# Optimization experiments

Measured on AMD Instinct MI355X. Metric: run time of the kernel, lower is better.

Reference implementation:

```python
import jax, jax.numpy as jnp
import numpy as np

C = 1024
KSIZE = 7
PAD = 3
STRIDE = 1


def _dwconv(x, w):
    # x: [B, C, L], w: [C, 1, K] depthwise (feature_group_count=C)
    return jax.lax.conv_general_dilated(
        x, w,
        window_strides=(STRIDE,),
        padding=[(PAD, PAD)],
        feature_group_count=C,
        dimension_numbers=('NCH', 'OIH', 'NCH'),
    )


def setup_inputs() -> dict:
    key = jax.random.key(0)
    kx, kq, kk, kv = jax.random.split(key, 4)
    B, L = 8, 4096
    x = jax.random.normal(kx, (B, C, L), dtype=jnp.float32)
    # depthwise conv weights, fan_in = 1*K per group -> kaiming-ish scale
    scale = 1.0 / np.sqrt(KSIZE)
    q_w = jax.random.normal(kq, (C, 1, KSIZE), dtype=jnp.float32) * scale
    k_w = jax.random.normal(kk, (C, 1, KSIZE), dtype=jnp.float32) * scale
    v_w = jax.random.normal(kv, (C, 1, KSIZE), dtype=jnp.float32) * scale
    return {"x": x, "q_w": q_w, "k_w": k_w, "v_w": v_w}


def reference(x, q_w, k_w, v_w):
    sqrt_dk = np.sqrt(C).astype(np.float32)
    q = _dwconv(x, q_w)  # [B, C, L']
    k = _dwconv(x, k_w)
    v = _dwconv(x, v_w)
    score = jnp.einsum('bcl,bdl->bcd', q, k) / sqrt_dk  # [B, C, C]
    attn = jax.nn.softmax(score, axis=-1)
    out = jnp.einsum('bcd,bdl->bcl', attn, v)  # [B, C, L']
    return out
```

## Files before the change

kernel.cpp:

```cpp
#include <hip/hip_runtime.h>
#include <hip/hip_bf16.h>

typedef unsigned short u16;
typedef __attribute__((ext_vector_type(8))) __bf16 bf16x8;
typedef __attribute__((ext_vector_type(4))) float f32x4;

#define CC 1024
#define LL 4096
#define NB 8

#define VMCNT(n) asm volatile("s_waitcnt vmcnt(" #n ")" ::: "memory")
#define LGKM0()  asm volatile("s_waitcnt lgkmcnt(0)" ::: "memory")

__device__ __forceinline__ u16 f2bf(float f) {
  union { float f; unsigned u; } v; v.f = f;
  unsigned u = v.u;
  return (u16)((u + 0x7fffu + ((u >> 16) & 1u)) >> 16);
}

__device__ __forceinline__ void gload_lds16(const void* g, void* l) {
  __builtin_amdgcn_global_load_lds(
      (const __attribute__((address_space(1))) void*)g,
      (__attribute__((address_space(3))) void*)l, 16, 0, 0);
}

__global__ __launch_bounds__(256) void dwconv_qkv(
    const float* __restrict__ x, const float* __restrict__ qw,
    const float* __restrict__ kw, const float* __restrict__ vw,
    u16* __restrict__ qo, u16* __restrict__ ko, u16* __restrict__ vto)
{
  __shared__ u16 vs[64][66];
  const int t  = threadIdx.x;
  const int l0 = blockIdx.x << 6;
  const int c0 = blockIdx.y << 6;
  const int b  = blockIdx.z;
  const int cc  = t >> 2;
  const int li0 = (t & 3) << 4;
  const int c   = c0 + cc;
  const float* xr = x + ((size_t)(b * CC + c)) * LL;
  const int p0 = l0 + li0;

  float xv[24];
  if (l0 != 0 && l0 != LL - 64) {
    const float4* base = (const float4*)(xr + p0 - 4);
#pragma unroll
    for (int j = 0; j < 6; ++j) {
      float4 f = base[j];
      xv[4 * j + 0] = f.x; xv[4 * j + 1] = f.y;
      xv[4 * j + 2] = f.z; xv[4 * j + 3] = f.w;
    }
  } else {
#pragma unroll
    for (int i = 0; i < 24; ++i) {
      int gl = p0 - 4 + i;
      xv[i] = ((unsigned)gl < (unsigned)LL) ? xr[gl] : 0.f;
    }
  }

  float wq[7], wk[7], wv[7];
#pragma unroll
  for (int j = 0; j < 7; ++j) {
    wq[j] = qw[c * 7 + j]; wk[j] = kw[c * 7 + j]; wv[j] = vw[c * 7 + j];
  }

  alignas(16) u16 qv[16], kv[16];
#pragma unroll
  for (int li = 0; li < 16; ++li) {
    float aq = 0.f, ak = 0.f, av = 0.f;
#pragma unroll
    for (int j = 0; j < 7; ++j) {
      float xf = xv[li + 1 + j];
      aq = fmaf(xf, wq[j], aq);
      ak = fmaf(xf, wk[j], ak);
      av = fmaf(xf, wv[j], av);
    }
    qv[li] = f2bf(aq);
    kv[li] = f2bf(ak);
    vs[li0 + li][cc] = f2bf(av);
  }
  size_t qoff = ((size_t)(b * CC + c)) * LL + p0;
  *(uint4*)(qo + qoff)     = ((const uint4*)qv)[0];
  *(uint4*)(qo + qoff + 8) = ((const uint4*)qv)[1];
  *(uint4*)(ko + qoff)     = ((const uint4*)kv)[0];
  *(uint4*)(ko + qoff + 8) = ((const uint4*)kv)[1];

  __syncthreads();
  const int ll = t >> 2;
  const int cg = (t & 3) << 4;
  alignas(16) u16 vr[16];
#pragma unroll
  for (int j = 0; j < 16; ++j) vr[j] = vs[ll][cg + j];
  size_t voff = ((size_t)(b * LL + l0 + ll)) * CC + c0 + cg;
  *(uint4*)(vto + voff)     = ((const uint4*)vr)[0];
  *(uint4*)(vto + voff + 8) = ((const uint4*)vr)[1];
}

__global__ __launch_bounds__(512, 2) void gemm256(
    const u16* __restrict__ A, int lda, size_t sA,
    const u16* __restrict__ B, int ldb, size_t sB,
    float* __restrict__ C0, float* __restrict__ C1, int ldc, size_t sC,
    int K, int ksplit)
{
  __shared__ alignas(16) u16 As[3][8192];
  __shared__ alignas(16) u16 Bs[3][8192];
  const int t    = threadIdx.x;
  const int lane = t & 63, wave = t >> 6;
  const int wrow = wave >> 2, wcol = wave & 3;
  const int bm = blockIdx.y << 8, bn = blockIdx.x << 8;
  const int bz = blockIdx.z;
  const int batch = (ksplit == 2) ? (bz >> 1) : bz;
  const int split = (ksplit == 2) ? (bz & 1) : 0;
  const int Ks    = (ksplit == 2) ? (K >> 1) : K;
  const u16* Ab = A + (size_t)batch * sA + split * Ks;
  const u16* Bb = B + (size_t)batch * sB + split * Ks;

  const int sc8  = (((lane & 3) ^ ((lane >> 3) & 3)) << 3);
  const int srow = lane >> 2;
  const u16* aSrcB[2]; const u16* bSrcB[2];
  int gdst[2];
#pragma unroll
  for (int i = 0; i < 2; ++i) {
    int g = wave * 2 + i;
    aSrcB[i] = Ab + (size_t)(bm + g * 16 + srow) * lda + sc8;
    bSrcB[i] = Bb + (size_t)(bn + g * 16 + srow) * ldb + sc8;
    gdst[i]  = g * 512;
  }

  const int r15 = lane & 15, kq = lane >> 4;
  int aOff[8], bOff[4];
#pragma unroll
  for (int m = 0; m < 8; ++m) {
    int r = wrow * 128 + m * 16 + r15;
    aOff[m] = r * 64 + ((kq ^ ((r >> 1) & 3)) << 4);
  }
#pragma unroll
  for (int n = 0; n < 4; ++n) {
    int r = wcol * 64 + n * 16 + r15;
    bOff[n] = r * 64 + ((kq ^ ((r >> 1) & 3)) << 4);
  }

  f32x4 acc[8][4];
#pragma unroll
  for (int i = 0; i < 8; ++i)
#pragma unroll
    for (int j = 0; j < 4; ++j) acc[i][j] = f32x4{0.f, 0.f, 0.f, 0.f};

  const int H = Ks >> 5;

#define STG_A(h2, s2) do {                                             \
    gload_lds16(aSrcB[0] + ((h2) << 5), &As[s2][gdst[0]]);             \
    gload_lds16(aSrcB[1] + ((h2) << 5), &As[s2][gdst[1]]); } while (0)
#define STG_B(h2, s2) do {                                             \
    gload_lds16(bSrcB[0] + ((h2) << 5), &Bs[s2][gdst[0]]);             \
    gload_lds16(bSrcB[1] + ((h2) << 5), &Bs[s2][gdst[1]]); } while (0)

  STG_A(0, 0); STG_B(0, 0);
  STG_A(1, 1); STG_B(1, 1);
  VMCNT(4);
  __builtin_amdgcn_s_barrier();

  int s = 0;
  for (int h = 0; h < H; ++h) {
    int s2 = s + 2; if (s2 >= 3) s2 -= 3;
    const char* Ap = (const char*)As[s];
    const char* Bp = (const char*)Bs[s];
    bf16x8 af0[4], bfr[4];
#pragma unroll
    for (int m = 0; m < 4; ++m) af0[m] = *(const bf16x8*)(Ap + aOff[m]);
#pragma unroll
    for (int n = 0; n < 4; ++n) bfr[n] = *(const bf16x8*)(Bp + bOff[n]);
    if (h + 2 < H) STG_A(h + 2, s2);
    __builtin_amdgcn_s_barrier();
    LGKM0();
    __builtin_amdgcn_sched_barrier(0);
    __builtin_amdgcn_s_setprio(1);
#pragma unroll
    for (int m = 0; m < 4; ++m)
#pragma unroll
      for (int n = 0; n < 4; ++n)
        acc[m][n] = __builtin_amdgcn_mfma_f32_16x16x32_bf16(
            af0[m], bfr[n], acc[m][n], 0, 0, 0);
    __builtin_amdgcn_s_setprio(0);
    __builtin_amdgcn_s_barrier();
    bf16x8 af1[4];
#pragma unroll
    for (int m = 0; m < 4; ++m) af1[m] = *(const bf16x8*)(Ap + aOff[m + 4]);
    if (h + 2 < H) STG_B(h + 2, s2);
    if (h < H - 2) { VMCNT(4); } else { VMCNT(0); }
    __builtin_amdgcn_s_barrier();
    LGKM0();
    __builtin_amdgcn_sched_barrier(0);
    __builtin_amdgcn_s_setprio(1);
#pragma unroll
    for (int m = 0; m < 4; ++m)
#pragma unroll
      for (int n = 0; n < 4; ++n)
        acc[m + 4][n] = __builtin_amdgcn_mfma_f32_16x16x32_bf16(
            af1[m], bfr[n], acc[m + 4][n], 0, 0, 0);
    __builtin_amdgcn_s_setprio(0);
    __builtin_amdgcn_s_barrier();
    s = s + 1; if (s == 3) s = 0;
  }
#undef STG_A
#undef STG_B

  float* Cb = (split ? C1 : C0) + (size_t)batch * sC;
  const int row0 = bm + wrow * 128 + kq * 4;
  const int col0 = bn + wcol * 64 + r15;
#pragma unroll
  for (int m = 0; m < 8; ++m)
#pragma unroll
    for (int n = 0; n < 4; ++n) {
      const int r   = row0 + m * 16;
      const int col = col0 + n * 16;
#pragma unroll
      for (int rr = 0; rr < 4; ++rr)
        Cb[(size_t)(r + rr) * ldc + col] = acc[m][n][rr];
    }
}

__global__ __launch_bounds__(256) void softmax_rows(
    float* __restrict__ score, const float* __restrict__ part)
{
  __shared__ float rmax[4], rsum[4];
  const int t = threadIdx.x;
  const int lane = t & 63, wv = t >> 6;
  float* sp = score + ((size_t)blockIdx.x << 10);
  const float* pp = part + ((size_t)blockIdx.x << 10);
  float4 v = ((const float4*)sp)[t];
  float4 w = ((const float4*)pp)[t];
  const float scale = 0.03125f;
  float a0 = (v.x + w.x) * scale, a1 = (v.y + w.y) * scale;
  float a2 = (v.z + w.z) * scale, a3 = (v.w + w.w) * scale;
  float m = fmaxf(fmaxf(a0, a1), fmaxf(a2, a3));
#pragma unroll
  for (int o = 1; o < 64; o <<= 1) m = fmaxf(m, __shfl_xor(m, o, 64));
  if (lane == 0) rmax[wv] = m;
  __syncthreads();
  m = fmaxf(fmaxf(rmax[0], rmax[1]), fmaxf(rmax[2], rmax[3]));
  float e0 = __expf(a0 - m), e1 = __expf(a1 - m);
  float e2 = __expf(a2 - m), e3 = __expf(a3 - m);
  float s = e0 + e1 + e2 + e3;
#pragma unroll
  for (int o = 1; o < 64; o <<= 1) s += __shfl_xor(s, o, 64);
  if (lane == 0) rsum[wv] = s;
  __syncthreads();
  s = rsum[0] + rsum[1] + rsum[2] + rsum[3];
  const float inv = 1.0f / s;
  union { u16 u[4]; uint2 p; } ob;
  ob.u[0] = f2bf(e0 * inv); ob.u[1] = f2bf(e1 * inv);
  ob.u[2] = f2bf(e2 * inv); ob.u[3] = f2bf(e3 * inv);
  *(uint2*)((u16*)sp + (t << 2)) = ob.p;
}

extern "C" void kernel_launch(void* const* d_in, const int* in_sizes, int n_in,
                              void* d_out, int out_size, void* d_ws, size_t ws_size,
                              hipStream_t stream) {
  const float* x  = (const float*)d_in[0];
  const float* qw = (const float*)d_in[1];
  const float* kw = (const float*)d_in[2];
  const float* vw = (const float*)d_in[3];
  float* out = (float*)d_out;
  char* ws = (char*)d_ws;

  u16*  q      = (u16*)ws;
  u16*  k      = (u16*)(ws + 67108864);
  u16*  vt     = (u16*)(ws + 134217728);
  float* score = (float*)(ws + 201326592);
  float* part  = out;

  dim3 cg(LL / 64, CC / 64, NB);
  dwconv_qkv<<<cg, 256, 0, stream>>>(x, qw, kw, vw, q, k, vt);

  dim3 g1(CC / 256, CC / 256, NB * 2);
  gemm256<<<g1, 512, 0, stream>>>(q, LL, (size_t)CC * LL,
                                  k, LL, (size_t)CC * LL,
                                  score, part, CC, (size_t)CC * CC, LL, 2);

  softmax_rows<<<NB * CC, 256, 0, stream>>>(score, part);

  dim3 g2(LL / 256, CC / 256, NB);
  gemm256<<<g2, 512, 0, stream>>>((const u16*)score, 2048, (size_t)CC * 2048,
                                  vt, CC, (size_t)LL * CC,
                                  out, nullptr, LL, (size_t)CC * LL, CC, 1);
}
```

Baseline: 286.9 us.

## Rework GEMM to 64-wide K tiles with double-buffered LDS and custom block mapping

Reorganizes the bf16 MFMA GEMM to stage 64-wide K slices into a 128KB double-buffered LDS region with an XOR swizzle. Global-to-LDS loads are split into quarter-tile chunks and interleaved between four MFMA phases, which removes the explicit lgkmcnt waits. Launches now use a flat 1D grid with a custom workgroup-to-tile mapping that groups batches/splits, aiming for better L2 locality. The single 128KB LDS buffer may limit occupancy to one block per CU despite the launch bounds. The barrier placement also carries race risk.

```diff
diff --git a/kernel.cpp b/kernel.cpp
--- a/kernel.cpp
+++ b/kernel.cpp
@@ -10,7 +10,7 @@
 #define NB 8
 
 #define VMCNT(n) asm volatile("s_waitcnt vmcnt(" #n ")" ::: "memory")
-#define LGKM0()  asm volatile("s_waitcnt lgkmcnt(0)" ::: "memory")
+#define BAR()    asm volatile("s_barrier" ::: "memory")
 
 __device__ __forceinline__ u16 f2bf(float f) {
   union { float f; unsigned u; } v; v.f = f;
@@ -95,49 +95,57 @@
   *(uint4*)(vto + voff + 8) = ((const uint4*)vr)[1];
 }
 
-__global__ __launch_bounds__(512, 2) void gemm256(
+__global__ __launch_bounds__(512, 2) void gemm256p(
     const u16* __restrict__ A, int lda, size_t sA,
     const u16* __restrict__ B, int ldb, size_t sB,
     float* __restrict__ C0, float* __restrict__ C1, int ldc, size_t sC,
-    int K, int ksplit)
+    int K, int ksplit, int mapmode)
 {
-  __shared__ alignas(16) u16 As[3][8192];
-  __shared__ alignas(16) u16 Bs[3][8192];
+  __shared__ alignas(16) u16 lds[65536];
   const int t    = threadIdx.x;
   const int lane = t & 63, wave = t >> 6;
   const int wrow = wave >> 2, wcol = wave & 3;
-  const int bm = blockIdx.y << 8, bn = blockIdx.x << 8;
-  const int bz = blockIdx.z;
-  const int batch = (ksplit == 2) ? (bz >> 1) : bz;
-  const int split = (ksplit == 2) ? (bz & 1) : 0;
+  int bx, by, z;
+  if (mapmode == 0) {
+    int wg = blockIdx.x; z = wg & 15; int r = wg >> 4; bx = r & 3; by = r >> 2;
+  } else {
+    int wg = blockIdx.x; z = wg & 7; by = (wg >> 3) & 3; bx = wg >> 5;
+  }
+  const int bm = by << 8, bn = bx << 8;
+  const int batch = (ksplit == 2) ? (z >> 1) : z;
+  const int split = (ksplit == 2) ? (z & 1) : 0;
   const int Ks    = (ksplit == 2) ? (K >> 1) : K;
-  const u16* Ab = A + (size_t)batch * sA + split * Ks;
-  const u16* Bb = B + (size_t)batch * sB + split * Ks;
-
-  const int sc8  = (((lane & 3) ^ ((lane >> 3) & 3)) << 3);
-  const int srow = lane >> 2;
-  const u16* aSrcB[2]; const u16* bSrcB[2];
-  int gdst[2];
+  const u16* Ab = A + (size_t)batch * sA + (size_t)split * Ks;
+  const u16* Bb = B + (size_t)batch * sB + (size_t)split * Ks;
+
+  const int srow = lane >> 3;
+  const int scol = ((lane & 7) ^ srow) << 3;
+  const u16* pA[2][2]; const u16* pB[2][2];
+  int dstOff[2];
 #pragma unroll
   for (int i = 0; i < 2; ++i) {
-    int g = wave * 2 + i;
-    aSrcB[i] = Ab + (size_t)(bm + g * 16 + srow) * lda + sc8;
-    bSrcB[i] = Bb + (size_t)(bn + g * 16 + srow) * ldb + sc8;
-    gdst[i]  = g * 512;
-  }
-
-  const int r15 = lane & 15, kq = lane >> 4;
-  int aOff[8], bOff[4];
-#pragma unroll
-  for (int m = 0; m < 8; ++m) {
-    int r = wrow * 128 + m * 16 + r15;
-    aOff[m] = r * 64 + ((kq ^ ((r >> 1) & 3)) << 4);
-  }
-#pragma unroll
-  for (int n = 0; n < 4; ++n) {
-    int r = wcol * 64 + n * 16 + r15;
-    bOff[n] = r * 64 + ((kq ^ ((r >> 1) & 3)) << 4);
-  }
+    int c = wave * 2 + i;
+    dstOff[i] = c * 1024 + lane * 16;
+    pA[0][i] = Ab + (size_t)(bm + c * 8 + srow) * lda + scol;
+    pA[1][i] = pA[0][i] + (size_t)128 * lda;
+    pB[0][i] = Bb + (size_t)(bn + c * 8 + srow) * ldb + scol;
+    pB[1][i] = pB[0][i] + (size_t)128 * ldb;
+  }
+
+#define STGH(P, h, base, koff)                                            \
+  do {                                                                    \
+    gload_lds16(P[h][0] + (koff), (char*)lds + (base) + dstOff[0]);       \
+    gload_lds16(P[h][1] + (koff), (char*)lds + (base) + dstOff[1]);       \
+  } while (0)
+
+  const int r15 = lane & 15, kq = lane >> 4, swz = r15 & 7;
+  int rowA[8], rowB[4], colK[2];
+#pragma unroll
+  for (int m = 0; m < 8; ++m) rowA[m] = (wrow * 128 + m * 16 + r15) * 128;
+#pragma unroll
+  for (int n = 0; n < 4; ++n) rowB[n] = 32768 + (wcol * 64 + n * 16 + r15) * 128;
+#pragma unroll
+  for (int s = 0; s < 2; ++s) colK[s] = (((s * 4 + kq) ^ swz)) << 4;
 
   f32x4 acc[8][4];
 #pragma unroll
@@ -145,64 +153,74 @@
 #pragma unroll
     for (int j = 0; j < 4; ++j) acc[i][j] = f32x4{0.f, 0.f, 0.f, 0.f};
 
-  const int H = Ks >> 5;
-
-#define STG_A(h2, s2) do {                                             \
-    gload_lds16(aSrcB[0] + ((h2) << 5), &As[s2][gdst[0]]);             \
-    gload_lds16(aSrcB[1] + ((h2) << 5), &As[s2][gdst[1]]); } while (0)
-#define STG_B(h2, s2) do {                                             \
-    gload_lds16(bSrcB[0] + ((h2) << 5), &Bs[s2][gdst[0]]);             \
-    gload_lds16(bSrcB[1] + ((h2) << 5), &Bs[s2][gdst[1]]); } while (0)
-
-  STG_A(0, 0); STG_B(0, 0);
-  STG_A(1, 1); STG_B(1, 1);
-  VMCNT(4);
-  __builtin_amdgcn_s_barrier();
-
-  int s = 0;
-  for (int h = 0; h < H; ++h) {
-    int s2 = s + 2; if (s2 >= 3) s2 -= 3;
-    const char* Ap = (const char*)As[s];
-    const char* Bp = (const char*)Bs[s];
-    bf16x8 af0[4], bfr[4];
-#pragma unroll
-    for (int m = 0; m < 4; ++m) af0[m] = *(const bf16x8*)(Ap + aOff[m]);
-#pragma unroll
-    for (int n = 0; n < 4; ++n) bfr[n] = *(const bf16x8*)(Bp + bOff[n]);
-    if (h + 2 < H) STG_A(h + 2, s2);
-    __builtin_amdgcn_s_barrier();
-    LGKM0();
-    __builtin_amdgcn_sched_barrier(0);
+  const int NT = Ks >> 6;
+
+  STGH(pA, 0, 0, 0);            STGH(pA, 1, 16384, 0);
+  STGH(pB, 0, 32768, 0);        STGH(pB, 1, 49152, 0);
+  STGH(pA, 0, 65536 + 0, 64);   STGH(pA, 1, 65536 + 16384, 64);
+  STGH(pB, 0, 65536 + 32768, 64);
+  VMCNT(6);
+  BAR();
+
+  const char* L = (const char*)lds;
+  for (int tt = 0; tt < NT; ++tt) {
+    const int d = tt & 1;
+    const int dbase = d << 16, sbase = (d ^ 1) << 16;
+    const int kN1 = (tt + 1) << 6, kN2 = (tt + 2) << 6;
+    bf16x8 a0[4], aK1a[4], b0[4];
+#pragma unroll
+    for (int m = 0; m < 4; ++m) {
+      a0[m]   = *(const bf16x8*)(L + dbase + rowA[m] + colK[0]);
+      aK1a[m] = *(const bf16x8*)(L + dbase + rowA[m] + colK[1]);
+    }
+#pragma unroll
+    for (int n = 0; n < 4; ++n) b0[n] = *(const bf16x8*)(L + dbase + rowB[n] + colK[0]);
+    if (tt + 1 < NT) STGH(pB, 1, sbase + 49152, kN1);
     __builtin_amdgcn_s_setprio(1);
 #pragma unroll
     for (int m = 0; m < 4; ++m)
 #pragma unroll
       for (int n = 0; n < 4; ++n)
-        acc[m][n] = __builtin_amdgcn_mfma_f32_16x16x32_bf16(
-            af0[m], bfr[n], acc[m][n], 0, 0, 0);
+        acc[m][n] = __builtin_amdgcn_mfma_f32_16x16x32_bf16(a0[m], b0[n], acc[m][n], 0, 0, 0);
     __builtin_amdgcn_s_setprio(0);
-    __builtin_amdgcn_s_barrier();
-    bf16x8 af1[4];
-#pragma unroll
-    for (int m = 0; m < 4; ++m) af1[m] = *(const bf16x8*)(Ap + aOff[m + 4]);
-    if (h + 2 < H) STG_B(h + 2, s2);
-    if (h < H - 2) { VMCNT(4); } else { VMCNT(0); }
-    __builtin_amdgcn_s_barrier();
-    LGKM0();
-    __builtin_amdgcn_sched_barrier(0);
+    bf16x8 a4[4], aK1b[4];
+#pragma unroll
+    for (int m = 0; m < 4; ++m) {
+      a4[m]   = *(const bf16x8*)(L + dbase + rowA[m + 4] + colK[0]);
+      aK1b[m] = *(const bf16x8*)(L + dbase + rowA[m + 4] + colK[1]);
+    }
     __builtin_amdgcn_s_setprio(1);
 #pragma unroll
     for (int m = 0; m < 4; ++m)
 #pragma unroll
       for (int n = 0; n < 4; ++n)
-        acc[m + 4][n] = __builtin_amdgcn_mfma_f32_16x16x32_bf16(
-            af1[m], bfr[n], acc[m + 4][n], 0, 0, 0);
+        acc[m + 4][n] = __builtin_amdgcn_mfma_f32_16x16x32_bf16(a4[m], b0[n], acc[m + 4][n], 0, 0, 0);
     __builtin_amdgcn_s_setprio(0);
-    __builtin_amdgcn_s_barrier();
-    s = s + 1; if (s == 3) s = 0;
-  }
-#undef STG_A
-#undef STG_B
+    BAR();
+    bf16x8 b1[4];
+#pragma unroll
+    for (int n = 0; n < 4; ++n) b1[n] = *(const bf16x8*)(L + dbase + rowB[n] + colK[1]);
+    if (tt + 2 < NT) STGH(pA, 0, dbase + 0, kN2);
+    __builtin_amdgcn_s_setprio(1);
+#pragma unroll
+    for (int m = 0; m < 4; ++m)
+#pragma unroll
+      for (int n = 0; n < 4; ++n)
+        acc[m][n] = __builtin_amdgcn_mfma_f32_16x16x32_bf16(aK1a[m], b1[n], acc[m][n], 0, 0, 0);
+    __builtin_amdgcn_s_setprio(0);
+    BAR();
+    if (tt + 2 < NT) { STGH(pA, 1, dbase + 16384, kN2); STGH(pB, 0, dbase + 32768, kN2); }
+    __builtin_amdgcn_s_setprio(1);
+#pragma unroll
+    for (int m = 0; m < 4; ++m)
+#pragma unroll
+      for (int n = 0; n < 4; ++n)
+        acc[m + 4][n] = __builtin_amdgcn_mfma_f32_16x16x32_bf16(aK1b[m], b1[n], acc[m + 4][n], 0, 0, 0);
+    __builtin_amdgcn_s_setprio(0);
+    if (tt < NT - 2) { VMCNT(6); } else { VMCNT(0); }
+    BAR();
+  }
+#undef STGH
 
   float* Cb = (split ? C1 : C0) + (size_t)batch * sC;
   const int row0 = bm + wrow * 128 + kq * 4;
@@ -272,15 +290,15 @@
   dim3 cg(LL / 64, CC / 64, NB);
   dwconv_qkv<<<cg, 256, 0, stream>>>(x, qw, kw, vw, q, k, vt);
 
-  dim3 g1(CC / 256, CC / 256, NB * 2);
-  gemm256<<<g1, 512, 0, stream>>>(q, LL, (size_t)CC * LL,
-                                  k, LL, (size_t)CC * LL,
-                                  score, part, CC, (size_t)CC * CC, LL, 2);
+  gemm256p<<<dim3(256), 512, 0, stream>>>(q, LL, (size_t)CC * LL,
+                                          k, LL, (size_t)CC * LL,
+                                          score, part, CC, (size_t)CC * CC,
+                                          LL, 2, 0);
 
   softmax_rows<<<NB * CC, 256, 0, stream>>>(score, part);
 
-  dim3 g2(LL / 256, CC / 256, NB);
-  gemm256<<<g2, 512, 0, stream>>>((const u16*)score, 2048, (size_t)CC * 2048,
-                                  vt, CC, (size_t)LL * CC,
-                                  out, nullptr, LL, (size_t)CC * LL, CC, 1);
-}
+  gemm256p<<<dim3(512), 512, 0, stream>>>((const u16*)score, 2048, (size_t)CC * 2048,
+                                          vt, CC, (size_t)LL * CC,
+                                          out, nullptr, LL, (size_t)CC * LL,
+                                          CC, 1, 1);
+}
```

Result: faster. 251.5 us (-12.3%).
